# Kernel tuning notes

Hardware: AMD Instinct MI355X
Metric: run time of the kernel (lower is better)

The kernel has to match this reference:

```python
import jax, jax.numpy as jnp
import numpy as np

DIM = 768
HEADS = 12
HEAD_DIM = DIM // HEADS  # 64
GRID = 48               # H = W = 48 tokens
RANK = 8                # LoRA rank


def setup_inputs() -> dict:
    key = jax.random.key(0)
    ks = jax.random.split(key, 20)
    s = 0.02
    inp = {
        "x": jax.random.normal(ks[0], (1, GRID, GRID, DIM), dtype=jnp.float32),
        "Wq": jax.random.normal(ks[1], (DIM, DIM), dtype=jnp.float32) * s,
        "bq": jax.random.normal(ks[2], (DIM,), dtype=jnp.float32) * s,
        "Wk": jax.random.normal(ks[3], (DIM, DIM), dtype=jnp.float32) * s,
        "bk": jax.random.normal(ks[4], (DIM,), dtype=jnp.float32) * s,
        "Wv": jax.random.normal(ks[5], (DIM, DIM), dtype=jnp.float32) * s,
        "bv": jax.random.normal(ks[6], (DIM,), dtype=jnp.float32) * s,
        "Wp": jax.random.normal(ks[7], (DIM, DIM), dtype=jnp.float32) * s,
        "bp": jax.random.normal(ks[8], (DIM,), dtype=jnp.float32) * s,
        "rel_pos_h": jax.random.normal(ks[9], (2 * GRID - 1, HEAD_DIM), dtype=jnp.float32) * s,
        "rel_pos_w": jax.random.normal(ks[10], (2 * GRID - 1, HEAD_DIM), dtype=jnp.float32) * s,
        "Aq": jax.random.normal(ks[11], (DIM, RANK), dtype=jnp.float32) * s,
        "Bq": jax.random.normal(ks[12], (RANK, DIM), dtype=jnp.float32) * s,
        "Ak": jax.random.normal(ks[13], (DIM, RANK), dtype=jnp.float32) * s,
        "Bk": jax.random.normal(ks[14], (RANK, DIM), dtype=jnp.float32) * s,
        "Av": jax.random.normal(ks[15], (DIM, RANK), dtype=jnp.float32) * s,
        "Bv": jax.random.normal(ks[16], (RANK, DIM), dtype=jnp.float32) * s,
    }
    return inp


def _get_rel_pos(size, rel_pos):
    # q_size == k_size == size, rel_pos has exactly 2*size-1 rows -> direct lookup
    idx = jnp.arange(size)[:, None] - jnp.arange(size)[None, :] + (size - 1)
    return rel_pos[idx]  # (size, size, head_dim)


def reference(x, Wq, bq, Wk, bk, Wv, bv, Wp, bp, rel_pos_h, rel_pos_w,
              Aq, Bq, Ak, Bk, Av, Bv):
    B, H, W, _ = x.shape
    N = H * W
    scale = HEAD_DIM ** -0.5

    # QKV projections + LoRA additions
    q = x @ Wq + bq + (x @ Aq) @ Bq
    k = x @ Wk + bk + (x @ Ak) @ Bk
    v = x @ Wv + bv + (x @ Av) @ Bv

    # (B, heads, N, head_dim)
    q = q.reshape(B, N, HEADS, HEAD_DIM).transpose(0, 2, 1, 3)
    k = k.reshape(B, N, HEADS, HEAD_DIM).transpose(0, 2, 1, 3)
    v = v.reshape(B, N, HEADS, HEAD_DIM).transpose(0, 2, 1, 3)

    attn = jnp.einsum('bhnc,bhmc->bhnm', q, k) * scale  # (B, heads, N, N)

    # Decomposed relative position bias (SAM add_decomposed_rel_pos)
    Rh = _get_rel_pos(H, rel_pos_h)  # (H, H, c)
    Rw = _get_rel_pos(W, rel_pos_w)  # (W, W, c)
    r_q = q.reshape(B, HEADS, H, W, HEAD_DIM)
    rel_h = jnp.einsum('bnhwc,hkc->bnhwk', r_q, Rh)  # (B, heads, H, W, H)
    rel_w = jnp.einsum('bnhwc,wkc->bnhwk', r_q, Rw)  # (B, heads, H, W, W)
    attn = (attn.reshape(B, HEADS, H, W, H, W)
            + rel_h[..., :, None] + rel_w[..., None, :]).reshape(B, HEADS, N, N)

    attn = jax.nn.softmax(attn, axis=-1)
    out = jnp.einsum('bhnm,bhmc->bhnc', attn, v)        # (B, heads, N, c)
    out = out.transpose(0, 2, 1, 3).reshape(B, H, W, DIM)
    return out @ Wp + bp
```

## Files before the change

kernel.cpp:

```cpp
#include <hip/hip_runtime.h>


#define DIM   768
#define HEADS 12
#define HD    64
#define NTOK  2304
#define RANK  8
#define GRD   48
#define CHUNKS 4
#define KTILES 9
#define LOG2E 1.44269504088896f

typedef __attribute__((ext_vector_type(8))) short bf16x8;
typedef __attribute__((ext_vector_type(4))) float f32x4;
typedef unsigned short ushort_t;

__device__ __forceinline__ unsigned short f2bf(float x) {
    union { float f; unsigned u; } v; v.f = x;
    unsigned r = v.u + 0x7fffu + ((v.u >> 16) & 1u);
    return (unsigned short)(r >> 16);
}

__global__ __launch_bounds__(256) void k_convert_x(
    const float* __restrict__ x, ushort_t* __restrict__ xb,
    const float* __restrict__ rph, const float* __restrict__ rpw,
    ushort_t* __restrict__ rphb, ushort_t* __restrict__ rpwb) {
    if (blockIdx.x < 1728) {
        int idx = (blockIdx.x * 256 + threadIdx.x) * 4;
        float4 v = *(const float4*)(x + idx);
        ushort4 o = make_ushort4(f2bf(v.x), f2bf(v.y), f2bf(v.z), f2bf(v.w));
        *(ushort4*)(xb + idx) = o;
    } else {
        int e = ((blockIdx.x - 1728) * 256 + threadIdx.x) * 4;
        const int TSZ = (2 * GRD - 1) * HD;
        if (e < TSZ) {
            float4 v = *(const float4*)(rph + e);
            ushort4 o = make_ushort4(f2bf(v.x), f2bf(v.y), f2bf(v.z), f2bf(v.w));
            *(ushort4*)(rphb + e) = o;
        } else if (e < 2 * TSZ) {
            float4 v = *(const float4*)(rpw + e - TSZ);
            ushort4 o = make_ushort4(f2bf(v.x), f2bf(v.y), f2bf(v.z), f2bf(v.w));
            *(ushort4*)(rpwb + e - TSZ) = o;
        }
    }
}

__global__ __launch_bounds__(256) void k_fold(
    const float* __restrict__ Wq, const float* __restrict__ Wk,
    const float* __restrict__ Wv, const float* __restrict__ Wp,
    const float* __restrict__ Aq, const float* __restrict__ Bq,
    const float* __restrict__ Ak, const float* __restrict__ Bk,
    const float* __restrict__ Av, const float* __restrict__ Bv,
    ushort_t* __restrict__ WT) {
    int kb = blockIdx.x * 32;
    int nb = blockIdx.y * 32;
    int qkv = nb / DIM;
    int nmod = nb % DIM;
    const float* W = (qkv == 0) ? Wq : (qkv == 1) ? Wk : (qkv == 2) ? Wv : Wp;
    const float* A = (qkv == 0) ? Aq : (qkv == 1) ? Ak : Av;
    const float* B = (qkv == 0) ? Bq : (qkv == 1) ? Bk : Bv;

    __shared__ float T[32][33];
    for (int i = threadIdx.x; i < 1024; i += 256) {
        int kl = i / 32, nl = i % 32;
        float v = W[(kb + kl) * DIM + nmod + nl];
        if (qkv < 3) {
            #pragma unroll
            for (int r = 0; r < RANK; r++)
                v += A[(kb + kl) * RANK + r] * B[r * DIM + nmod + nl];
        }
        T[kl][nl] = v;
    }
    __syncthreads();
    for (int i = threadIdx.x; i < 1024; i += 256) {
        int nl = i / 32, kl = i % 32;
        WT[(size_t)(nb + nl) * DIM + kb + kl] = f2bf(T[kl][nl]);
    }
}

__global__ __launch_bounds__(256) void k_gemm_qkv(
    const ushort_t* __restrict__ xb, const ushort_t* __restrict__ WT,
    const float* __restrict__ bq, const float* __restrict__ bk,
    const float* __restrict__ bv,
    ushort_t* __restrict__ Qb, ushort_t* __restrict__ Kb,
    ushort_t* __restrict__ Vtb) {
    __shared__ __align__(16) ushort_t As[128 * 40];
    __shared__ __align__(16) ushort_t Bs[128 * 40];
    int tid = threadIdx.x;
    int wave = tid >> 6, lane = tid & 63, quad = lane >> 4, l16 = lane & 15;
    int wx = wave & 1, wy = wave >> 1;
    int nb = blockIdx.x * 128, mb = blockIdx.y * 128;

    f32x4 zero = {0.f, 0.f, 0.f, 0.f};
    f32x4 acc[4][4];
    #pragma unroll
    for (int i = 0; i < 4; i++)
        #pragma unroll
        for (int j = 0; j < 4; j++) acc[i][j] = zero;

    const ushort_t* Ag = xb + (size_t)(mb + (tid >> 1)) * DIM + (tid & 1) * 16;
    const ushort_t* Bg = WT + (size_t)(nb + (tid >> 1)) * DIM + (tid & 1) * 16;
    int sidx = (tid >> 1) * 40 + (tid & 1) * 16;

    for (int k0 = 0; k0 < DIM; k0 += 32) {
        uint4 a0 = *(const uint4*)(Ag + k0);
        uint4 a1 = *(const uint4*)(Ag + k0 + 8);
        uint4 b0 = *(const uint4*)(Bg + k0);
        uint4 b1 = *(const uint4*)(Bg + k0 + 8);
        __syncthreads();
        *(uint4*)&As[sidx] = a0;  *(uint4*)&As[sidx + 8] = a1;
        *(uint4*)&Bs[sidx] = b0;  *(uint4*)&Bs[sidx + 8] = b1;
        __syncthreads();
        bf16x8 af[4], bf[4];
        #pragma unroll
        for (int i = 0; i < 4; i++)
            af[i] = *(const bf16x8*)&As[(wy * 64 + i * 16 + l16) * 40 + quad * 8];
        #pragma unroll
        for (int j = 0; j < 4; j++)
            bf[j] = *(const bf16x8*)&Bs[(wx * 64 + j * 16 + l16) * 40 + quad * 8];
        #pragma unroll
        for (int i = 0; i < 4; i++)
            #pragma unroll
            for (int j = 0; j < 4; j++)
                acc[i][j] = __builtin_amdgcn_mfma_f32_16x16x32_bf16(af[i], bf[j], acc[i][j], 0, 0, 0);
    }

    #pragma unroll
    for (int j = 0; j < 4; j++) {
        int col = nb + wx * 64 + j * 16 + l16;
        int qkv = col / DIM, rem = col % DIM;
        int hh = rem >> 6, cc = rem & 63;
        const float* bias = (qkv == 0) ? bq : (qkv == 1) ? bk : bv;
        float bval = bias[rem];
        #pragma unroll
        for (int i = 0; i < 4; i++) {
            #pragma unroll
            for (int r = 0; r < 4; r++) {
                int row = mb + wy * 64 + i * 16 + quad * 4 + r;
                unsigned short o = f2bf(acc[i][j][r] + bval);
                if (qkv == 0)      Qb[(size_t)(hh * NTOK + row) * HD + cc] = o;
                else if (qkv == 1) Kb[(size_t)(hh * NTOK + row) * HD + cc] = o;
                else               Vtb[(size_t)(hh * HD + cc) * NTOK + row] = o;
            }
        }
    }
}

__global__ __launch_bounds__(256) void k_relmm(
    const ushort_t* __restrict__ Qb, const ushort_t* __restrict__ rphb,
    const ushort_t* __restrict__ rpwb, float* __restrict__ relH,
    float* __restrict__ relW) {
    int id = blockIdx.x * 4 + (threadIdx.x >> 6);
    int lane = threadIdx.x & 63, quad = lane >> 4, l16 = lane & 15;
    bool isW = id >= 576;
    int t = isW ? id - 576 : id;
    int h = t / GRD, g = t % GRD;
    const ushort_t* tab = isW ? rpwb : rphb;
    float* outp = isW ? relW : relH;

    f32x4 zero = {0.f, 0.f, 0.f, 0.f};
    f32x4 acc[3][3];
    #pragma unroll
    for (int i = 0; i < 3; i++)
        #pragma unroll
        for (int j = 0; j < 3; j++) acc[i][j] = zero;

    bf16x8 bfr[3][2];
    #pragma unroll
    for (int ct = 0; ct < 3; ct++) {
        int trow = g + 47 - (ct * 16 + l16);
        bfr[ct][0] = *(const bf16x8*)&tab[(size_t)trow * HD + quad * 8];
        bfr[ct][1] = *(const bf16x8*)&tab[(size_t)trow * HD + 32 + quad * 8];
    }
    #pragma unroll
    for (int ms = 0; ms < 3; ms++) {
        int m = ms * 16 + l16;
        int n = isW ? m * GRD + g : g * GRD + m;
        bf16x8 a0 = *(const bf16x8*)&Qb[(size_t)(h * NTOK + n) * HD + quad * 8];
        bf16x8 a1 = *(const bf16x8*)&Qb[(size_t)(h * NTOK + n) * HD + 32 + quad * 8];
        #pragma unroll
        for (int ct = 0; ct < 3; ct++) {
            acc[ms][ct] = __builtin_amdgcn_mfma_f32_16x16x32_bf16(a0, bfr[ct][0], acc[ms][ct], 0, 0, 0);
            acc[ms][ct] = __builtin_amdgcn_mfma_f32_16x16x32_bf16(a1, bfr[ct][1], acc[ms][ct], 0, 0, 0);
        }
    }
    #pragma unroll
    for (int ms = 0; ms < 3; ms++) {
        #pragma unroll
        for (int ct = 0; ct < 3; ct++) {
            #pragma unroll
            for (int r = 0; r < 4; r++) {
                int m = ms * 16 + quad * 4 + r;
                int n = isW ? m * GRD + g : g * GRD + m;
                int col = ct * 16 + l16;
                outp[(size_t)(h * NTOK + n) * GRD + col] = acc[ms][ct][r] * LOG2E;
            }
        }
    }
}

__global__ __launch_bounds__(256) void k_attn(
    const ushort_t* __restrict__ Qb, const ushort_t* __restrict__ Kb,
    const ushort_t* __restrict__ Vtb, const float* __restrict__ relH,
    const float* __restrict__ relW, float* __restrict__ Opart,
    float* __restrict__ Lpart) {
    int qt = blockIdx.x, h = blockIdx.y, chunk = blockIdx.z;
    int tid = threadIdx.x;
    int wave = tid >> 6, lane = tid & 63, quad = lane >> 4, l16 = lane & 15;
    int qbase = qt * 128;
    int kbase = chunk * (KTILES * 64);

    __shared__ __align__(16) ushort_t Ks[64 * 72];
    __shared__ __align__(16) ushort_t Vs[64 * 72];
    __shared__ __align__(16) ushort_t Ps[4][32 * 72];
    __shared__ float rhs[128 * 13];

    bf16x8 qf[2][2];
    #pragma unroll
    for (int s = 0; s < 2; s++) {
        int qrow = qbase + wave * 32 + s * 16 + l16;
        qf[s][0] = *(const bf16x8*)&Qb[(size_t)(h * NTOK + qrow) * HD + quad * 8];
        qf[s][1] = *(const bf16x8*)&Qb[(size_t)(h * NTOK + qrow) * HD + 32 + quad * 8];
    }

    float rwreg[2][4][3];
    #pragma unroll
    for (int s = 0; s < 2; s++)
        #pragma unroll
        for (int r = 0; r < 4; r++) {
            int row = qbase + wave * 32 + s * 16 + quad * 4 + r;
            #pragma unroll
            for (int j = 0; j < 3; j++)
                rwreg[s][r][j] = relW[(size_t)(h * NTOK + row) * GRD + j * 16 + l16];
        }

    for (int i = tid; i < 128 * 12; i += 256) {
        int r = i / 12, c = i % 12;
        rhs[r * 13 + c] = relH[(size_t)(h * NTOK + qbase + r) * GRD + chunk * 12 + c];
    }

    float l_st[2][4] = {{0.f,0.f,0.f,0.f},{0.f,0.f,0.f,0.f}};
    f32x4 zero = {0.f, 0.f, 0.f, 0.f};
    f32x4 oacc[2][4];
    #pragma unroll
    for (int s = 0; s < 2; s++)
        #pragma unroll
        for (int j = 0; j < 4; j++) oacc[s][j] = zero;

    const float scale2 = 0.125f * LOG2E;
    int stg_r = tid >> 2, stg_c = (tid & 3) * 16;
    const ushort_t* Kg = Kb + (size_t)(h * NTOK + stg_r) * HD + stg_c;
    const ushort_t* Vg = Vtb + (size_t)(h * HD + stg_r) * NTOK + stg_c;

    uint4 rk0, rk1, rv0, rv1;
    {
        int kb = kbase;
        rk0 = *(const uint4*)(Kg + (size_t)kb * HD);
        rk1 = *(const uint4*)(Kg + (size_t)kb * HD + 8);
        rv0 = *(const uint4*)(Vg + kb);
        rv1 = *(const uint4*)(Vg + kb + 8);
    }

    for (int kt = 0; kt < KTILES; kt++) {
        __syncthreads();
        *(uint4*)&Ks[stg_r * 72 + stg_c]     = rk0;
        *(uint4*)&Ks[stg_r * 72 + stg_c + 8] = rk1;
        *(uint4*)&Vs[stg_r * 72 + stg_c]     = rv0;
        *(uint4*)&Vs[stg_r * 72 + stg_c + 8] = rv1;
        __syncthreads();

        {
            int ktn = (kt + 1 < KTILES) ? kt + 1 : kt;
            int kb = kbase + ktn * 64;
            rk0 = *(const uint4*)(Kg + (size_t)kb * HD);
            rk1 = *(const uint4*)(Kg + (size_t)kb * HD + 8);
            rv0 = *(const uint4*)(Vg + kb);
            rv1 = *(const uint4*)(Vg + kb + 8);
        }

        f32x4 sv[2][4];
        #pragma unroll
        for (int ct = 0; ct < 4; ct++) {
            bf16x8 kf0 = *(const bf16x8*)&Ks[(ct * 16 + l16) * 72 + quad * 8];
            bf16x8 kf1 = *(const bf16x8*)&Ks[(ct * 16 + l16) * 72 + 32 + quad * 8];
            #pragma unroll
            for (int s = 0; s < 2; s++) {
                f32x4 z = zero;
                z = __builtin_amdgcn_mfma_f32_16x16x32_bf16(qf[s][0], kf0, z, 0, 0, 0);
                z = __builtin_amdgcn_mfma_f32_16x16x32_bf16(qf[s][1], kf1, z, 0, 0, 0);
                sv[s][ct] = z;
            }
        }

        #pragma unroll
        for (int ct = 0; ct < 4; ct++) {
            int m = 4 * kt + ct;
            int khl = m / 3;
            int j = m % 3;
            #pragma unroll
            for (int s = 0; s < 2; s++) {
                #pragma unroll
                for (int r = 0; r < 4; r++) {
                    int rloc = wave * 32 + s * 16 + quad * 4 + r;
                    float v = sv[s][ct][r] * scale2 + rhs[rloc * 13 + khl] + rwreg[s][r][j];
                    float p = __builtin_amdgcn_exp2f(v);
                    l_st[s][r] += p;
                    Ps[wave][(s * 16 + quad * 4 + r) * 72 + ct * 16 + l16] = f2bf(p);
                }
            }
        }

        bf16x8 pf[2][2];
        #pragma unroll
        for (int s = 0; s < 2; s++) {
            pf[s][0] = *(const bf16x8*)&Ps[wave][(s * 16 + l16) * 72 + quad * 8];
            pf[s][1] = *(const bf16x8*)&Ps[wave][(s * 16 + l16) * 72 + 32 + quad * 8];
        }
        #pragma unroll
        for (int ct = 0; ct < 4; ct++) {
            bf16x8 vf0 = *(const bf16x8*)&Vs[(ct * 16 + l16) * 72 + quad * 8];
            bf16x8 vf1 = *(const bf16x8*)&Vs[(ct * 16 + l16) * 72 + 32 + quad * 8];
            #pragma unroll
            for (int s = 0; s < 2; s++) {
                oacc[s][ct] = __builtin_amdgcn_mfma_f32_16x16x32_bf16(pf[s][0], vf0, oacc[s][ct], 0, 0, 0);
                oacc[s][ct] = __builtin_amdgcn_mfma_f32_16x16x32_bf16(pf[s][1], vf1, oacc[s][ct], 0, 0, 0);
            }
        }
    }

    #pragma unroll
    for (int s = 0; s < 2; s++)
        #pragma unroll
        for (int r = 0; r < 4; r++) {
            float l = l_st[s][r];
            l += __shfl_xor(l, 1);
            l += __shfl_xor(l, 2);
            l += __shfl_xor(l, 4);
            l += __shfl_xor(l, 8);
            l_st[s][r] = l;
        }

    size_t obase = (size_t)(chunk * HEADS + h) * NTOK;
    #pragma unroll
    for (int s = 0; s < 2; s++) {
        #pragma unroll
        for (int ct = 0; ct < 4; ct++) {
            #pragma unroll
            for (int r = 0; r < 4; r++) {
                int row = qbase + wave * 32 + s * 16 + quad * 4 + r;
                Opart[(obase + row) * HD + ct * 16 + l16] = oacc[s][ct][r];
            }
        }
        if (l16 == 0) {
            #pragma unroll
            for (int r = 0; r < 4; r++) {
                int row = qbase + wave * 32 + s * 16 + quad * 4 + r;
                Lpart[obase + row] = l_st[s][r];
            }
        }
    }
}

__global__ __launch_bounds__(256) void k_merge(const float* __restrict__ Opart,
                                               const float* __restrict__ Lpart,
                                               ushort_t* __restrict__ Ob) {
    int t = blockIdx.x * 256 + threadIdx.x;
    int e = t * 4;
    int c = e & (HD - 1);
    int row = (e >> 6) % NTOK;
    int h = e / (NTOK * HD);
    const int ostride = HEADS * NTOK * HD;
    float4 s = {0.f, 0.f, 0.f, 0.f};
    float l = 0.f;
    #pragma unroll
    for (int ch = 0; ch < CHUNKS; ch++) {
        float4 v = *(const float4*)&Opart[(size_t)ch * ostride + e];
        s.x += v.x; s.y += v.y; s.z += v.z; s.w += v.w;
        l += Lpart[(size_t)(ch * HEADS + h) * NTOK + row];
    }
    float inv = 1.0f / l;
    ushort4 o = make_ushort4(f2bf(s.x * inv), f2bf(s.y * inv),
                             f2bf(s.z * inv), f2bf(s.w * inv));
    *(ushort4*)&Ob[(size_t)row * DIM + h * HD + c] = o;
}

__global__ __launch_bounds__(256) void k_gemm_proj(
    const ushort_t* __restrict__ Ob, const ushort_t* __restrict__ WTp,
    const float* __restrict__ bp, float* __restrict__ out) {
    __shared__ __align__(16) ushort_t As[128 * 40];
    __shared__ __align__(16) ushort_t Bs[128 * 40];
    int tid = threadIdx.x;
    int wave = tid >> 6, lane = tid & 63, quad = lane >> 4, l16 = lane & 15;
    int wx = wave & 1, wy = wave >> 1;
    int nb = blockIdx.x * 128, mb = blockIdx.y * 128;

    f32x4 zero = {0.f, 0.f, 0.f, 0.f};
    f32x4 acc[4][4];
    #pragma unroll
    for (int i = 0; i < 4; i++)
        #pragma unroll
        for (int j = 0; j < 4; j++) acc[i][j] = zero;

    const ushort_t* Ag = Ob + (size_t)(mb + (tid >> 1)) * DIM + (tid & 1) * 16;
    const ushort_t* Bg = WTp + (size_t)(nb + (tid >> 1)) * DIM + (tid & 1) * 16;
    int sidx = (tid >> 1) * 40 + (tid & 1) * 16;

    for (int k0 = 0; k0 < DIM; k0 += 32) {
        uint4 a0 = *(const uint4*)(Ag + k0);
        uint4 a1 = *(const uint4*)(Ag + k0 + 8);
        uint4 b0 = *(const uint4*)(Bg + k0);
        uint4 b1 = *(const uint4*)(Bg + k0 + 8);
        __syncthreads();
        *(uint4*)&As[sidx] = a0;  *(uint4*)&As[sidx + 8] = a1;
        *(uint4*)&Bs[sidx] = b0;  *(uint4*)&Bs[sidx + 8] = b1;
        __syncthreads();
        bf16x8 af[4], bf[4];
        #pragma unroll
        for (int i = 0; i < 4; i++)
            af[i] = *(const bf16x8*)&As[(wy * 64 + i * 16 + l16) * 40 + quad * 8];
        #pragma unroll
        for (int j = 0; j < 4; j++)
            bf[j] = *(const bf16x8*)&Bs[(wx * 64 + j * 16 + l16) * 40 + quad * 8];
        #pragma unroll
        for (int i = 0; i < 4; i++)
            #pragma unroll
            for (int j = 0; j < 4; j++)
                acc[i][j] = __builtin_amdgcn_mfma_f32_16x16x32_bf16(af[i], bf[j], acc[i][j], 0, 0, 0);
    }

    #pragma unroll
    for (int j = 0; j < 4; j++) {
        int col = nb + wx * 64 + j * 16 + l16;
        float bval = bp[col];
        #pragma unroll
        for (int i = 0; i < 4; i++) {
            #pragma unroll
            for (int r = 0; r < 4; r++) {
                int row = mb + wy * 64 + i * 16 + quad * 4 + r;
                out[(size_t)row * DIM + col] = acc[i][j][r] + bval;
            }
        }
    }
}

extern "C" void kernel_launch(void* const* d_in, const int* in_sizes, int n_in,
                              void* d_out, int out_size, void* d_ws, size_t ws_size,
                              hipStream_t stream) {
    const float* x   = (const float*)d_in[0];
    const float* Wq  = (const float*)d_in[1];
    const float* bq  = (const float*)d_in[2];
    const float* Wk  = (const float*)d_in[3];
    const float* bk  = (const float*)d_in[4];
    const float* Wv  = (const float*)d_in[5];
    const float* bv  = (const float*)d_in[6];
    const float* Wp  = (const float*)d_in[7];
    const float* bp  = (const float*)d_in[8];
    const float* rph = (const float*)d_in[9];
    const float* rpw = (const float*)d_in[10];
    const float* Aq  = (const float*)d_in[11];
    const float* Bq  = (const float*)d_in[12];
    const float* Ak  = (const float*)d_in[13];
    const float* Bk  = (const float*)d_in[14];
    const float* Av  = (const float*)d_in[15];
    const float* Bv  = (const float*)d_in[16];
    float* out = (float*)d_out;

    char* w = (char*)d_ws;
    size_t off = 0;
    auto carve = [&](size_t bytes) {
        char* p = w + off;
        off += (bytes + 255) & ~(size_t)255;
        return p;
    };
    ushort_t* xb    = (ushort_t*)carve((size_t)NTOK * DIM * 2);
    ushort_t* WT    = (ushort_t*)carve((size_t)4 * DIM * DIM * 2);
    ushort_t* Qb    = (ushort_t*)carve((size_t)HEADS * NTOK * HD * 2);
    ushort_t* Kb    = (ushort_t*)carve((size_t)HEADS * NTOK * HD * 2);
    ushort_t* Vtb   = (ushort_t*)carve((size_t)HEADS * HD * NTOK * 2);
    float*    relH  = (float*)carve((size_t)HEADS * NTOK * GRD * 4);
    float*    relW  = (float*)carve((size_t)HEADS * NTOK * GRD * 4);
    ushort_t* Ob    = (ushort_t*)carve((size_t)NTOK * DIM * 2);
    float*    Opart = (float*)carve((size_t)CHUNKS * HEADS * NTOK * HD * 4);
    float*    Lpart = (float*)carve((size_t)CHUNKS * HEADS * NTOK * 4);
    ushort_t* rphb  = (ushort_t*)carve((size_t)(2 * GRD - 1) * HD * 2);
    ushort_t* rpwb  = (ushort_t*)carve((size_t)(2 * GRD - 1) * HD * 2);

    k_convert_x<<<dim3(1728 + 12), dim3(256), 0, stream>>>(x, xb, rph, rpw, rphb, rpwb);
    k_fold<<<dim3(DIM / 32, 4 * DIM / 32), dim3(256), 0, stream>>>(
        Wq, Wk, Wv, Wp, Aq, Bq, Ak, Bk, Av, Bv, WT);
    k_gemm_qkv<<<dim3(18, 18), dim3(256), 0, stream>>>(
        xb, WT, bq, bk, bv, Qb, Kb, Vtb);
    k_relmm<<<dim3(288), dim3(256), 0, stream>>>(
        Qb, rphb, rpwb, relH, relW);
    k_attn<<<dim3(NTOK / 128, HEADS, CHUNKS), dim3(256), 0, stream>>>(
        Qb, Kb, Vtb, relH, relW, Opart, Lpart);
    k_merge<<<dim3(HEADS * NTOK * HD / (256 * 4)), dim3(256), 0, stream>>>(
        Opart, Lpart, Ob);
    k_gemm_proj<<<dim3(6, 18), dim3(256), 0, stream>>>(
        Ob, WT + (size_t)3 * DIM * DIM, bp, out);
}
```

Measured before the change: 216.0 us.

## Transpose attention score MFMA, stage rel-pos bias in LDS as bf16, use direct-to-LDS loads in QKV GEMM

The attention kernel now computes S^T (K as the A operand), so each lane holds four consecutive key scores for one query row. This lets the bias be read as packed bf16 pairs from LDS, the probabilities be packed with perm and written to LDS as 8-byte stores, and the row-sum reduction shrink to two shuffles. The LDS padding and the grid order change so that the heads and chunks sharing a query tile launch together. Separately, the QKV GEMM switches to global_load_lds direct-to-LDS loads with unpadded tiles. The costs are possible LDS bank conflicts in the GEMM and reduced precision in the bias terms.

```diff
diff --git a/kernel.cpp b/kernel.cpp
--- a/kernel.cpp
+++ b/kernel.cpp
@@ -8,7 +8,6 @@
 #define RANK  8
 #define GRD   48
 #define CHUNKS 4
-#define KTILES 9
 #define LOG2E 1.44269504088896f
 
 typedef __attribute__((ext_vector_type(8))) short bf16x8;
@@ -19,6 +18,15 @@
     union { float f; unsigned u; } v; v.f = x;
     unsigned r = v.u + 0x7fffu + ((v.u >> 16) & 1u);
     return (unsigned short)(r >> 16);
+}
+__device__ __forceinline__ float bf2f(unsigned short h) {
+    return __uint_as_float(((unsigned)h) << 16);
+}
+
+__device__ __forceinline__ void gload_lds16(const ushort_t* g, ushort_t* l) {
+    __builtin_amdgcn_global_load_lds(
+        (const __attribute__((address_space(1))) unsigned int*)g,
+        (__attribute__((address_space(3))) unsigned int*)l, 16, 0, 0);
 }
 
 __global__ __launch_bounds__(256) void k_convert_x(
@@ -84,8 +92,8 @@
     const float* __restrict__ bv,
     ushort_t* __restrict__ Qb, ushort_t* __restrict__ Kb,
     ushort_t* __restrict__ Vtb) {
-    __shared__ __align__(16) ushort_t As[128 * 40];
-    __shared__ __align__(16) ushort_t Bs[128 * 40];
+    __shared__ __align__(16) ushort_t As[128 * 32];
+    __shared__ __align__(16) ushort_t Bs[128 * 32];
     int tid = threadIdx.x;
     int wave = tid >> 6, lane = tid & 63, quad = lane >> 4, l16 = lane & 15;
     int wx = wave & 1, wy = wave >> 1;
@@ -98,26 +106,27 @@
         #pragma unroll
         for (int j = 0; j < 4; j++) acc[i][j] = zero;
 
-    const ushort_t* Ag = xb + (size_t)(mb + (tid >> 1)) * DIM + (tid & 1) * 16;
-    const ushort_t* Bg = WT + (size_t)(nb + (tid >> 1)) * DIM + (tid & 1) * 16;
-    int sidx = (tid >> 1) * 40 + (tid & 1) * 16;
+    int rl = lane >> 2;
+    int cl = (lane & 3) * 8;
+    const ushort_t* gA = xb + (size_t)(mb + wave * 32 + rl) * DIM + cl;
+    const ushort_t* gB = WT + (size_t)(nb + wave * 32 + rl) * DIM + cl;
+    ushort_t* lA = &As[(wave * 32) * 32];
+    ushort_t* lB = &Bs[(wave * 32) * 32];
 
     for (int k0 = 0; k0 < DIM; k0 += 32) {
-        uint4 a0 = *(const uint4*)(Ag + k0);
-        uint4 a1 = *(const uint4*)(Ag + k0 + 8);
-        uint4 b0 = *(const uint4*)(Bg + k0);
-        uint4 b1 = *(const uint4*)(Bg + k0 + 8);
-        __syncthreads();
-        *(uint4*)&As[sidx] = a0;  *(uint4*)&As[sidx + 8] = a1;
-        *(uint4*)&Bs[sidx] = b0;  *(uint4*)&Bs[sidx + 8] = b1;
+        __syncthreads();
+        gload_lds16(gA + k0,            lA);
+        gload_lds16(gA + k0 + 16 * DIM, lA + 16 * 32);
+        gload_lds16(gB + k0,            lB);
+        gload_lds16(gB + k0 + 16 * DIM, lB + 16 * 32);
         __syncthreads();
         bf16x8 af[4], bf[4];
         #pragma unroll
         for (int i = 0; i < 4; i++)
-            af[i] = *(const bf16x8*)&As[(wy * 64 + i * 16 + l16) * 40 + quad * 8];
+            af[i] = *(const bf16x8*)&As[(wy * 64 + i * 16 + l16) * 32 + quad * 8];
         #pragma unroll
         for (int j = 0; j < 4; j++)
-            bf[j] = *(const bf16x8*)&Bs[(wx * 64 + j * 16 + l16) * 40 + quad * 8];
+            bf[j] = *(const bf16x8*)&Bs[(wx * 64 + j * 16 + l16) * 32 + quad * 8];
         #pragma unroll
         for (int i = 0; i < 4; i++)
             #pragma unroll
@@ -204,16 +213,26 @@
     const ushort_t* __restrict__ Vtb, const float* __restrict__ relH,
     const float* __restrict__ relW, float* __restrict__ Opart,
     float* __restrict__ Lpart) {
-    int qt = blockIdx.x, h = blockIdx.y, chunk = blockIdx.z;
+    int h = blockIdx.x >> 2, chunk = blockIdx.x & 3, qt = blockIdx.y;
     int tid = threadIdx.x;
     int wave = tid >> 6, lane = tid & 63, quad = lane >> 4, l16 = lane & 15;
     int qbase = qt * 128;
-    int kbase = chunk * (KTILES * 64);
-
-    __shared__ __align__(16) ushort_t Ks[64 * 72];
-    __shared__ __align__(16) ushort_t Vs[64 * 72];
-    __shared__ __align__(16) ushort_t Ps[4][32 * 72];
-    __shared__ float rhs[128 * 13];
+    int kbase = chunk * 576;
+
+    __shared__ __align__(16) ushort_t Ks[64 * 68];
+    __shared__ __align__(16) ushort_t Vs[64 * 68];
+    __shared__ __align__(16) ushort_t Ps[4][32 * 68];
+    __shared__ __align__(16) ushort_t rws[128 * 52];
+    __shared__ __align__(16) ushort_t rhs[128 * 14];
+
+    for (int i = tid; i < 128 * 48; i += 256) {
+        int r = i / 48, c = i % 48;
+        rws[r * 52 + c] = f2bf(relW[(size_t)(h * NTOK + qbase + r) * GRD + c]);
+    }
+    for (int i = tid; i < 128 * 12; i += 256) {
+        int r = i / 12, c = i % 12;
+        rhs[r * 14 + c] = f2bf(relH[(size_t)(h * NTOK + qbase + r) * GRD + chunk * 12 + c]);
+    }
 
     bf16x8 qf[2][2];
     #pragma unroll
@@ -223,141 +242,114 @@
         qf[s][1] = *(const bf16x8*)&Qb[(size_t)(h * NTOK + qrow) * HD + 32 + quad * 8];
     }
 
-    float rwreg[2][4][3];
-    #pragma unroll
-    for (int s = 0; s < 2; s++)
-        #pragma unroll
-        for (int r = 0; r < 4; r++) {
-            int row = qbase + wave * 32 + s * 16 + quad * 4 + r;
-            #pragma unroll
-            for (int j = 0; j < 3; j++)
-                rwreg[s][r][j] = relW[(size_t)(h * NTOK + row) * GRD + j * 16 + l16];
-        }
-
-    for (int i = tid; i < 128 * 12; i += 256) {
-        int r = i / 12, c = i % 12;
-        rhs[r * 13 + c] = relH[(size_t)(h * NTOK + qbase + r) * GRD + chunk * 12 + c];
-    }
-
-    float l_st[2][4] = {{0.f,0.f,0.f,0.f},{0.f,0.f,0.f,0.f}};
+    int r0 = tid >> 3, c0 = (tid & 7) * 8;
+    const ushort_t* kg0 = Kb + (size_t)(h * NTOK + r0) * HD + c0;
+    const ushort_t* kg1 = Kb + (size_t)(h * NTOK + r0 + 32) * HD + c0;
+    const ushort_t* vg0 = Vtb + (size_t)(h * HD + r0) * NTOK + c0;
+    const ushort_t* vg1 = Vtb + (size_t)(h * HD + r0 + 32) * NTOK + c0;
+    int sk0 = r0 * 68 + c0, sk1 = sk0 + 32 * 68;
+
+    float lacc[2] = {0.f, 0.f};
     f32x4 zero = {0.f, 0.f, 0.f, 0.f};
     f32x4 oacc[2][4];
     #pragma unroll
     for (int s = 0; s < 2; s++)
         #pragma unroll
-        for (int j = 0; j < 4; j++) oacc[s][j] = zero;
+        for (int cs = 0; cs < 4; cs++) oacc[s][cs] = zero;
 
     const float scale2 = 0.125f * LOG2E;
-    int stg_r = tid >> 2, stg_c = (tid & 3) * 16;
-    const ushort_t* Kg = Kb + (size_t)(h * NTOK + stg_r) * HD + stg_c;
-    const ushort_t* Vg = Vtb + (size_t)(h * HD + stg_r) * NTOK + stg_c;
-
-    uint4 rk0, rk1, rv0, rv1;
-    {
-        int kb = kbase;
-        rk0 = *(const uint4*)(Kg + (size_t)kb * HD);
-        rk1 = *(const uint4*)(Kg + (size_t)kb * HD + 8);
-        rv0 = *(const uint4*)(Vg + kb);
-        rv1 = *(const uint4*)(Vg + kb + 8);
-    }
-
-    for (int kt = 0; kt < KTILES; kt++) {
-        __syncthreads();
-        *(uint4*)&Ks[stg_r * 72 + stg_c]     = rk0;
-        *(uint4*)&Ks[stg_r * 72 + stg_c + 8] = rk1;
-        *(uint4*)&Vs[stg_r * 72 + stg_c]     = rv0;
-        *(uint4*)&Vs[stg_r * 72 + stg_c + 8] = rv1;
-        __syncthreads();
-
-        {
-            int ktn = (kt + 1 < KTILES) ? kt + 1 : kt;
-            int kb = kbase + ktn * 64;
-            rk0 = *(const uint4*)(Kg + (size_t)kb * HD);
-            rk1 = *(const uint4*)(Kg + (size_t)kb * HD + 8);
-            rv0 = *(const uint4*)(Vg + kb);
-            rv1 = *(const uint4*)(Vg + kb + 8);
-        }
-
-        f32x4 sv[2][4];
-        #pragma unroll
-        for (int ct = 0; ct < 4; ct++) {
-            bf16x8 kf0 = *(const bf16x8*)&Ks[(ct * 16 + l16) * 72 + quad * 8];
-            bf16x8 kf1 = *(const bf16x8*)&Ks[(ct * 16 + l16) * 72 + 32 + quad * 8];
+
+    uint4 rk0 = *(const uint4*)(kg0 + (size_t)kbase * HD);
+    uint4 rk1 = *(const uint4*)(kg1 + (size_t)kbase * HD);
+    uint4 rv0 = *(const uint4*)(vg0 + kbase);
+    uint4 rv1 = *(const uint4*)(vg1 + kbase);
+
+    for (int kt = 0; kt < 9; kt++) {
+        int kb = kbase + kt * 64;
+        __syncthreads();
+        *(uint4*)&Ks[sk0] = rk0;  *(uint4*)&Ks[sk1] = rk1;
+        *(uint4*)&Vs[sk0] = rv0;  *(uint4*)&Vs[sk1] = rv1;
+        __syncthreads();
+        if (kt < 8) {
+            int kbn = kb + 64;
+            rk0 = *(const uint4*)(kg0 + (size_t)kbn * HD);
+            rk1 = *(const uint4*)(kg1 + (size_t)kbn * HD);
+            rv0 = *(const uint4*)(vg0 + kbn);
+            rv1 = *(const uint4*)(vg1 + kbn);
+        }
+
+        #pragma unroll
+        for (int ks = 0; ks < 4; ks++) {
+            bf16x8 kf0 = *(const bf16x8*)&Ks[(ks * 16 + l16) * 68 + quad * 8];
+            bf16x8 kf1 = *(const bf16x8*)&Ks[(ks * 16 + l16) * 68 + 32 + quad * 8];
+            f32x4 st[2];
             #pragma unroll
             for (int s = 0; s < 2; s++) {
                 f32x4 z = zero;
-                z = __builtin_amdgcn_mfma_f32_16x16x32_bf16(qf[s][0], kf0, z, 0, 0, 0);
-                z = __builtin_amdgcn_mfma_f32_16x16x32_bf16(qf[s][1], kf1, z, 0, 0, 0);
-                sv[s][ct] = z;
-            }
-        }
-
-        #pragma unroll
-        for (int ct = 0; ct < 4; ct++) {
-            int m = 4 * kt + ct;
-            int khl = m / 3;
-            int j = m % 3;
+                z = __builtin_amdgcn_mfma_f32_16x16x32_bf16(kf0, qf[s][0], z, 0, 0, 0);
+                z = __builtin_amdgcn_mfma_f32_16x16x32_bf16(kf1, qf[s][1], z, 0, 0, 0);
+                st[s] = z;
+            }
+            int kb4 = kb + ks * 16 + quad * 4;
+            int kh = kb4 / 48;
+            int khl = kh - chunk * 12;
+            int kw0 = kb4 - kh * 48;
             #pragma unroll
             for (int s = 0; s < 2; s++) {
-                #pragma unroll
-                for (int r = 0; r < 4; r++) {
-                    int rloc = wave * 32 + s * 16 + quad * 4 + r;
-                    float v = sv[s][ct][r] * scale2 + rhs[rloc * 13 + khl] + rwreg[s][r][j];
-                    float p = __builtin_amdgcn_exp2f(v);
-                    l_st[s][r] += p;
-                    Ps[wave][(s * 16 + quad * 4 + r) * 72 + ct * 16 + l16] = f2bf(p);
-                }
-            }
-        }
-
-        bf16x8 pf[2][2];
+                int row = wave * 32 + s * 16 + l16;
+                float rh = bf2f(rhs[row * 14 + khl]);
+                uint2 u = *(const uint2*)&rws[row * 52 + kw0];
+                float p0 = __builtin_amdgcn_exp2f(st[s][0] * scale2 + rh + __uint_as_float(u.x << 16));
+                float p1 = __builtin_amdgcn_exp2f(st[s][1] * scale2 + rh + __uint_as_float(u.x & 0xffff0000u));
+                float p2 = __builtin_amdgcn_exp2f(st[s][2] * scale2 + rh + __uint_as_float(u.y << 16));
+                float p3 = __builtin_amdgcn_exp2f(st[s][3] * scale2 + rh + __uint_as_float(u.y & 0xffff0000u));
+                lacc[s] += (p0 + p1) + (p2 + p3);
+                uint2 w;
+                w.x = __builtin_amdgcn_perm(__float_as_uint(p1), __float_as_uint(p0), 0x07060302u);
+                w.y = __builtin_amdgcn_perm(__float_as_uint(p3), __float_as_uint(p2), 0x07060302u);
+                *(uint2*)&Ps[wave][(s * 16 + l16) * 68 + ks * 16 + quad * 4] = w;
+            }
+        }
+
+        bf16x8 vf[4][2];
+        #pragma unroll
+        for (int cs = 0; cs < 4; cs++) {
+            vf[cs][0] = *(const bf16x8*)&Vs[(cs * 16 + l16) * 68 + quad * 8];
+            vf[cs][1] = *(const bf16x8*)&Vs[(cs * 16 + l16) * 68 + 32 + quad * 8];
+        }
         #pragma unroll
         for (int s = 0; s < 2; s++) {
-            pf[s][0] = *(const bf16x8*)&Ps[wave][(s * 16 + l16) * 72 + quad * 8];
-            pf[s][1] = *(const bf16x8*)&Ps[wave][(s * 16 + l16) * 72 + 32 + quad * 8];
-        }
-        #pragma unroll
-        for (int ct = 0; ct < 4; ct++) {
-            bf16x8 vf0 = *(const bf16x8*)&Vs[(ct * 16 + l16) * 72 + quad * 8];
-            bf16x8 vf1 = *(const bf16x8*)&Vs[(ct * 16 + l16) * 72 + 32 + quad * 8];
-            #pragma unroll
-            for (int s = 0; s < 2; s++) {
-                oacc[s][ct] = __builtin_amdgcn_mfma_f32_16x16x32_bf16(pf[s][0], vf0, oacc[s][ct], 0, 0, 0);
-                oacc[s][ct] = __builtin_amdgcn_mfma_f32_16x16x32_bf16(pf[s][1], vf1, oacc[s][ct], 0, 0, 0);
-            }
-        }
-    }
-
-    #pragma unroll
-    for (int s = 0; s < 2; s++)
-        #pragma unroll
-        for (int r = 0; r < 4; r++) {
-            float l = l_st[s][r];
-            l += __shfl_xor(l, 1);
-            l += __shfl_xor(l, 2);
-            l += __shfl_xor(l, 4);
-            l += __shfl_xor(l, 8);
-            l_st[s][r] = l;
-        }
+            bf16x8 pa0 = *(const bf16x8*)&Ps[wave][(s * 16 + l16) * 68 + quad * 8];
+            bf16x8 pa1 = *(const bf16x8*)&Ps[wave][(s * 16 + l16) * 68 + 32 + quad * 8];
+            #pragma unroll
+            for (int cs = 0; cs < 4; cs++) {
+                oacc[s][cs] = __builtin_amdgcn_mfma_f32_16x16x32_bf16(pa0, vf[cs][0], oacc[s][cs], 0, 0, 0);
+                oacc[s][cs] = __builtin_amdgcn_mfma_f32_16x16x32_bf16(pa1, vf[cs][1], oacc[s][cs], 0, 0, 0);
+            }
+        }
+    }
+
+    #pragma unroll
+    for (int s = 0; s < 2; s++) {
+        float l = lacc[s];
+        l += __shfl_xor(l, 16);
+        l += __shfl_xor(l, 32);
+        lacc[s] = l;
+    }
 
     size_t obase = (size_t)(chunk * HEADS + h) * NTOK;
     #pragma unroll
     for (int s = 0; s < 2; s++) {
         #pragma unroll
-        for (int ct = 0; ct < 4; ct++) {
+        for (int cs = 0; cs < 4; cs++) {
             #pragma unroll
             for (int r = 0; r < 4; r++) {
                 int row = qbase + wave * 32 + s * 16 + quad * 4 + r;
-                Opart[(obase + row) * HD + ct * 16 + l16] = oacc[s][ct][r];
-            }
-        }
-        if (l16 == 0) {
-            #pragma unroll
-            for (int r = 0; r < 4; r++) {
-                int row = qbase + wave * 32 + s * 16 + quad * 4 + r;
-                Lpart[obase + row] = l_st[s][r];
-            }
-        }
+                Opart[(obase + row) * HD + cs * 16 + l16] = oacc[s][cs][r];
+            }
+        }
+        if (quad == 0)
+            Lpart[obase + qbase + wave * 32 + s * 16 + l16] = lacc[s];
     }
 }
 
@@ -492,7 +484,7 @@
         xb, WT, bq, bk, bv, Qb, Kb, Vtb);
     k_relmm<<<dim3(288), dim3(256), 0, stream>>>(
         Qb, rphb, rpwb, relH, relW);
-    k_attn<<<dim3(NTOK / 128, HEADS, CHUNKS), dim3(256), 0, stream>>>(
+    k_attn<<<dim3(HEADS * CHUNKS, NTOK / 128), dim3(256), 0, stream>>>(
         Qb, Kb, Vtb, relH, relW, Opart, Lpart);
     k_merge<<<dim3(HEADS * NTOK * HD / (256 * 4)), dim3(256), 0, stream>>>(
         Opart, Lpart, Ob);
```

Result: no change. 213.6 us (-1.1%).
